# Kernel optimization log

Measured on AMD Instinct MI355X. Metric: run time of the kernel, lower is better.

## Reference

```python
import jax, jax.numpy as jnp
import numpy as np

B, C, H, W = 8, 256, 48, 48
CK = 64  # C // k
WSCALE = 0.3 / np.sqrt(C)  # keep exp(QK^T) finite (original has no 1/sqrt(d) scaling)


def conv1x1(x, w, b):
    # x: (B,C,H,W), w: (O,C,1,1), b: (O,) -> (B,O,H,W)
    return jnp.einsum('bchw,oc->bohw', x, w[:, :, 0, 0]) + b[None, :, None, None]


def setup_inputs() -> dict:
    key = jax.random.key(0)
    ks = jax.random.split(key, 6)
    x = jax.random.normal(ks[0], (B, C, H, W), dtype=jnp.float32)
    qw = jax.random.normal(ks[1], (CK, C, 1, 1), dtype=jnp.float32) * WSCALE
    kw = jax.random.normal(ks[2], (CK, C, 1, 1), dtype=jnp.float32) * WSCALE
    vw = jax.random.normal(ks[3], (C, C, 1, 1), dtype=jnp.float32) * (1.0 / np.sqrt(C))
    gw = jax.random.normal(ks[4], (C, C, 1, 1), dtype=jnp.float32) * (1.0 / np.sqrt(C))
    zk = jnp.zeros((CK,), dtype=jnp.float32)
    zc = jnp.zeros((C,), dtype=jnp.float32)
    return {
        'x': x,
        'query_weight': qw, 'query_bias': zk,
        'key_weight': kw, 'key_bias': zk,
        'value_weight': vw, 'value_bias': zc,
        'gamma_weight': gw, 'gamma_bias': zc,
        'k': 4,
    }


def reference(x, query_weight, query_bias, key_weight, key_bias,
              value_weight, value_bias, gamma_weight, gamma_bias, k):
    b, c, h, w = x.shape
    n = h * w
    q = conv1x1(x, query_weight, query_bias).reshape(b, -1, n)   # (B,Ck,N)
    kk = conv1x1(x, key_weight, key_bias).reshape(b, -1, n)      # (B,Ck,N)
    # energy[b,i,j] = q_i . k_j  (queries on rows, no sqrt(d) scaling)
    energy = jnp.einsum('bci,bcj->bij', q, kk)                   # (B,N,N)
    energy = jnp.exp(energy)
    energy = energy / jnp.sum(energy, axis=2, keepdims=True)     # unnormalized-softmax over keys
    v = conv1x1(x, value_weight, value_bias).reshape(b, c, n)    # (B,C,N)
    # out[b,c,j] = sum_i v[b,c,i] * energy[b,i,j]  (faithful to torch.bmm(V, energy))
    out = jnp.einsum('bci,bij->bcj', v, energy).reshape(b, c, h, w)
    out = conv1x1(out, gamma_weight, gamma_bias)
    return out
```

## Files before the change

kernel.cpp:

```cpp
#include <hip/hip_runtime.h>

#define BATCH 8
#define CIN   256
#define NPIX  2304
#define CKD   64
#define QKLD  128
#define NJT   (NPIX / 16)
#define NIC   (NPIX / 32)
#define KSPL  4
#define ICPS  (NIC / KSPL)
#define NJB   (NPIX / 64)

typedef _Float16 f16;
typedef __attribute__((ext_vector_type(4))) _Float16 f16x4;
typedef __attribute__((ext_vector_type(8))) _Float16 f16x8;
typedef __attribute__((ext_vector_type(4))) float    f32x4;

__global__ __launch_bounds__(256) void cast_w(
    const float* __restrict__ qw, const float* __restrict__ kw,
    const float* __restrict__ vw, const float* __restrict__ gw,
    f16* __restrict__ Wqk, f16* __restrict__ Wv, f16* __restrict__ Wg)
{
    int idx = (blockIdx.x * 256 + threadIdx.x) * 4;
    const float* src;
    f16* dst;
    if (idx < 16384)      { src = qw + idx;           dst = Wqk + idx; }
    else if (idx < 32768) { src = kw + (idx - 16384); dst = Wqk + idx; }
    else if (idx < 98304) { src = vw + (idx - 32768); dst = Wv + (idx - 32768); }
    else                  { src = gw + (idx - 98304); dst = Wg + (idx - 98304); }
    float4 v = *(const float4*)src;
    f16x4 h = { (f16)v.x, (f16)v.y, (f16)v.z, (f16)v.w };
    *(f16x4*)dst = h;
}

__global__ __launch_bounds__(256) void cast_xT(
    const float* __restrict__ x, f16* __restrict__ xT)
{
    __shared__ float s[64][65];
    const int t = threadIdx.x;
    const int n0 = blockIdx.x * 64, c0 = blockIdx.y * 64, b = blockIdx.z;
    const float* xb = x + ((size_t)b * CIN + c0) * NPIX + n0;

    const int cl = t >> 4, ng = (t & 15) * 4;
    #pragma unroll
    for (int p = 0; p < 4; ++p) {
        float4 v = *(const float4*)(xb + (size_t)(cl + 16 * p) * NPIX + ng);
        s[cl + 16 * p][ng + 0] = v.x;
        s[cl + 16 * p][ng + 1] = v.y;
        s[cl + 16 * p][ng + 2] = v.z;
        s[cl + 16 * p][ng + 3] = v.w;
    }
    __syncthreads();
    const int nl = t >> 2, cs = (t & 3) * 16;
    f16 h[16];
    #pragma unroll
    for (int j = 0; j < 16; ++j) h[j] = (f16)s[cs + j][nl];
    f16* gp = &xT[((size_t)b * NPIX + n0 + nl) * CIN + c0 + cs];
    *(f16x8*)gp       = *(f16x8*)&h[0];
    *(f16x8*)(gp + 8) = *(f16x8*)&h[8];
}

__global__ __launch_bounds__(256) void qk_conv_mfma(
    const f16* __restrict__ xT, const f16* __restrict__ Wqk,
    const float* __restrict__ qbias, const float* __restrict__ kbias,
    f16* __restrict__ qkT)
{
    const int t = threadIdx.x, w = t >> 6, lane = t & 63;
    const int quad = lane >> 4, l16 = lane & 15;
    const int wm = w & 1, wn = w >> 1;
    const int n0 = blockIdx.x * 32, b = blockIdx.y;

    const f16* bp = xT + ((size_t)b * NPIX + n0 + 16 * wn + l16) * CIN;
    const f16* ap = Wqk + (size_t)(64 * wm + l16) * CIN;

    f32x4 acc[4];
    #pragma unroll
    for (int mt = 0; mt < 4; ++mt) acc[mt] = (f32x4){0.f, 0.f, 0.f, 0.f};

    #pragma unroll
    for (int kk = 0; kk < CIN; kk += 32) {
        f16x8 bf = *(const f16x8*)(bp + kk + quad * 8);
        #pragma unroll
        for (int mt = 0; mt < 4; ++mt) {
            f16x8 af = *(const f16x8*)(ap + (size_t)mt * 16 * CIN + kk + quad * 8);
            acc[mt] = __builtin_amdgcn_mfma_f32_16x16x32_f16(af, bf, acc[mt], 0, 0, 0);
        }
    }
    const int n = n0 + 16 * wn + l16;
    const float* bias = wm ? kbias - 64 : qbias;
    #pragma unroll
    for (int mt = 0; mt < 4; ++mt) {
        int ob = 64 * wm + 16 * mt + quad * 4;
        f16x4 h;
        #pragma unroll
        for (int r = 0; r < 4; ++r)
            h[r] = (f16)(acc[mt][r] + bias[ob + r]);
        *(f16x4*)&qkT[((size_t)b * NPIX + n) * QKLD + ob] = h;
    }
}

#define ESL 136
__global__ __launch_bounds__(256) void energy_mfma(
    const f16* __restrict__ qkT, float* __restrict__ Pred,
    f16* __restrict__ Et_blk)
{
    __shared__ __align__(16) f16 es[64 * ESL];
    __shared__ float red2[2][128];
    const int t    = threadIdx.x;
    const int w    = t >> 6, lane = t & 63;
    const int quad = lane >> 4, l16 = lane & 15;
    const int j0 = blockIdx.x * 64, i0 = blockIdx.y * 128, b = blockIdx.z;
    const f16* base = qkT + (size_t)b * NPIX * QKLD;

    f32x4 acc[8];
    #pragma unroll
    for (int mt = 0; mt < 8; ++mt) acc[mt] = (f32x4){0.f, 0.f, 0.f, 0.f};

    #pragma unroll
    for (int ks = 0; ks < 2; ++ks) {
        f16x8 bf = *(const f16x8*)&base[(size_t)(j0 + 16 * w + l16) * QKLD + 64 + ks * 32 + quad * 8];
        #pragma unroll
        for (int mt = 0; mt < 8; ++mt) {
            f16x8 af = *(const f16x8*)&base[(size_t)(i0 + 16 * mt + l16) * QKLD + ks * 32 + quad * 8];
            acc[mt] = __builtin_amdgcn_mfma_f32_16x16x32_f16(af, bf, acc[mt], 0, 0, 0);
        }
    }

    #pragma unroll
    for (int mt = 0; mt < 8; ++mt) {
        f16x4 h = { (f16)__expf(acc[mt][0]), (f16)__expf(acc[mt][1]),
                    (f16)__expf(acc[mt][2]), (f16)__expf(acc[mt][3]) };
        *(f16x4*)&es[(16 * w + l16) * ESL + 16 * mt + quad * 4] = h;
    }
    __syncthreads();

    #pragma unroll
    for (int p = 0; p < 4; ++p) {
        int g  = t + 256 * p;
        int jt = g >> 8, ic = (g >> 6) & 3, ln = g & 63;
        f16x8 v = *(const f16x8*)&es[(jt * 16 + (ln & 15)) * ESL + ic * 32 + (ln >> 4) * 8];
        *(f16x8*)&Et_blk[(((size_t)b * NJT + (j0 >> 4) + jt) * NIC + (i0 >> 5) + ic) * 512 + ln * 8] = v;
    }

    {
        int i = t & 127, jq = t >> 7;
        float s = 0.f;
        #pragma unroll
        for (int jj = 0; jj < 32; ++jj)
            s += (float)es[(jq * 32 + jj) * ESL + i];
        red2[jq][i] = s;
    }
    __syncthreads();
    if (t < 128) {
        Pred[((size_t)b * NPIX + i0 + t) * NJB + blockIdx.x] =
            red2[0][t] + red2[1][t];
    }
}

__global__ __launch_bounds__(256) void reduce_S(
    const float* __restrict__ Pred, float* __restrict__ S)
{
    int idx = blockIdx.x * 256 + threadIdx.x;
    const float* p = Pred + (size_t)idx * NJB;
    float s = 0.f;
    #pragma unroll
    for (int x = 0; x < NJB; x += 4) {
        float4 v = *(const float4*)(p + x);
        s += v.x + v.y + v.z + v.w;
    }
    S[idx] = s;
}

__global__ __launch_bounds__(256) void v_conv_mfma(
    const f16* __restrict__ xT, const f16* __restrict__ Wv,
    const float* __restrict__ vbias, const float* __restrict__ S,
    f16* __restrict__ u_blk)
{
    __shared__ __align__(16) f16 smem[9216];
    f16* As = smem;
    f16* Bs = smem + 128 * 40;
    f16* us = smem;
    const int t = threadIdx.x, w = t >> 6, lane = t & 63;
    const int quad = lane >> 4, l16 = lane & 15;
    const int wm = w & 1, wn = w >> 1;
    const int i0 = blockIdx.x * 64, c0 = blockIdx.y * 128, b = blockIdx.z;
    const int sub = t >> 2, le = t & 3;
    const f16* srcA = Wv + (size_t)(c0 + sub) * CIN + le * 8;
    const f16* srcB = xT + ((size_t)b * NPIX + i0 + sub) * CIN + le * 8;
    const int ldsw = sub * 40 + le * 8;

    f32x4 acc[4][2];
    #pragma unroll
    for (int mt = 0; mt < 4; ++mt)
        #pragma unroll
        for (int nt = 0; nt < 2; ++nt)
            acc[mt][nt] = (f32x4){0.f, 0.f, 0.f, 0.f};

    for (int kk = 0; kk < CIN; kk += 32) {
        f16x8 ta0 = *(const f16x8*)(srcA + kk);
        f16x8 ta1 = *(const f16x8*)(srcA + (size_t)64 * CIN + kk);
        f16x8 tb0 = *(const f16x8*)(srcB + kk);
        __syncthreads();
        *(f16x8*)&As[ldsw]           = ta0;
        *(f16x8*)&As[64 * 40 + ldsw] = ta1;
        *(f16x8*)&Bs[ldsw]           = tb0;
        __syncthreads();
        f16x8 af[4], bf[2];
        #pragma unroll
        for (int mt = 0; mt < 4; ++mt)
            af[mt] = *(const f16x8*)&As[(64 * wm + 16 * mt + l16) * 40 + quad * 8];
        #pragma unroll
        for (int nt = 0; nt < 2; ++nt)
            bf[nt] = *(const f16x8*)&Bs[(32 * wn + 16 * nt + l16) * 40 + quad * 8];
        #pragma unroll
        for (int mt = 0; mt < 4; ++mt)
            #pragma unroll
            for (int nt = 0; nt < 2; ++nt)
                acc[mt][nt] = __builtin_amdgcn_mfma_f32_16x16x32_f16(
                    af[mt], bf[nt], acc[mt][nt], 0, 0, 0);
    }

    __syncthreads();
    #pragma unroll
    for (int nt = 0; nt < 2; ++nt) {
        int i = 32 * wn + 16 * nt + l16;
        float is = 1.0f / S[(size_t)b * NPIX + i0 + i];
        #pragma unroll
        for (int mt = 0; mt < 4; ++mt)
            #pragma unroll
            for (int r = 0; r < 4; ++r) {
                int c = 64 * wm + 16 * mt + quad * 4 + r;
                us[c * 72 + i] = (f16)((acc[mt][nt][r] + vbias[c0 + c]) * is);
            }
    }
    __syncthreads();
    #pragma unroll
    for (int p = 0; p < 4; ++p) {
        int g  = t + 256 * p;
        int ct = g >> 7, ic = (g >> 6) & 1, ln = g & 63;
        f16x8 v = *(const f16x8*)&us[(ct * 16 + (ln & 15)) * 72 + ic * 32 + (ln >> 4) * 8];
        *(f16x8*)&u_blk[(((size_t)b * 16 + (c0 >> 4) + ct) * NIC + (i0 >> 5) + ic) * 512 + ln * 8] = v;
    }
}

__global__ __launch_bounds__(512) void bmm_mfma(
    const f16* __restrict__ u_blk, const f16* __restrict__ Et_blk,
    f16* __restrict__ p0, f16* __restrict__ p1,
    f16* __restrict__ p2, f16* __restrict__ p3)
{
    const int t = threadIdx.x, w = t >> 6, lane = t & 63;
    const int quad = lane >> 4, l16 = lane & 15;
    const int wc = w & 3, wj = w >> 2;
    const int j0 = blockIdx.x * 128;
    const int ks = blockIdx.y, b = blockIdx.z;
    const f16* ub  = u_blk  + (size_t)b * 16 * NIC * 512 + (size_t)lane * 8;
    const f16* ebb = Et_blk + (size_t)b * NJT * NIC * 512 + (size_t)lane * 8;
    f16* outp = (ks == 0) ? p0 : (ks == 1 ? p1 : (ks == 2 ? p2 : p3));
    const int jtb = (j0 >> 4) + wj * 4;

    f32x4 acc[4][4];
    #pragma unroll
    for (int mt = 0; mt < 4; ++mt)
        #pragma unroll
        for (int nt = 0; nt < 4; ++nt)
            acc[mt][nt] = (f32x4){0.f, 0.f, 0.f, 0.f};

    const int ic0 = ks * ICPS;
    #pragma unroll 2
    for (int ic = ic0; ic < ic0 + ICPS; ++ic) {
        f16x8 af[4], bf[4];
        #pragma unroll
        for (int mt = 0; mt < 4; ++mt)
            af[mt] = *(const f16x8*)(ub + (size_t)((wc * 4 + mt) * NIC + ic) * 512);
        #pragma unroll
        for (int nt = 0; nt < 4; ++nt)
            bf[nt] = *(const f16x8*)(ebb + (size_t)((jtb + nt) * NIC + ic) * 512);
        #pragma unroll
        for (int mt = 0; mt < 4; ++mt)
            #pragma unroll
            for (int nt = 0; nt < 4; ++nt)
                acc[mt][nt] = __builtin_amdgcn_mfma_f32_16x16x32_f16(
                    af[mt], bf[nt], acc[mt][nt], 0, 0, 0);
    }

    #pragma unroll
    for (int mt = 0; mt < 4; ++mt) {
        int cb = (wc * 4 + mt) * 16 + quad * 4;
        #pragma unroll
        for (int nt = 0; nt < 4; ++nt) {
            int j = j0 + (wj * 4 + nt) * 16 + l16;
            f16x4 h = { (f16)acc[mt][nt][0], (f16)acc[mt][nt][1],
                        (f16)acc[mt][nt][2], (f16)acc[mt][nt][3] };
            *(f16x4*)&outp[((size_t)b * NPIX + j) * CIN + cb] = h;
        }
    }
}

__global__ __launch_bounds__(256) void gamma_conv_mfma(
    const f16* __restrict__ p0, const f16* __restrict__ p1,
    const f16* __restrict__ p2, const f16* __restrict__ p3,
    const f16* __restrict__ Wg, const float* __restrict__ gbias,
    float* __restrict__ out)
{
    __shared__ __align__(16) f16 As[128 * 40];
    __shared__ __align__(16) f16 Bs[64 * 40];
    const int t = threadIdx.x, w = t >> 6, lane = t & 63;
    const int quad = lane >> 4, l16 = lane & 15;
    const int wm = w & 1, wn = w >> 1;
    const int j0 = blockIdx.x * 64, o0 = blockIdx.y * 128, b = blockIdx.z;
    const int sub = t >> 2, le = t & 3;
    const f16* srcA  = Wg + (size_t)(o0 + sub) * CIN + le * 8;
    const size_t boff = ((size_t)b * NPIX + j0 + sub) * CIN + le * 8;
    const int ldsw = sub * 40 + le * 8;

    f32x4 acc[4][2];
    #pragma unroll
    for (int mt = 0; mt < 4; ++mt)
        #pragma unroll
        for (int nt = 0; nt < 2; ++nt)
            acc[mt][nt] = (f32x4){0.f, 0.f, 0.f, 0.f};

    for (int kk = 0; kk < CIN; kk += 32) {
        f16x8 ta0 = *(const f16x8*)(srcA + kk);
        f16x8 ta1 = *(const f16x8*)(srcA + (size_t)64 * CIN + kk);
        f16x8 tb0 = *(const f16x8*)(p0 + boff + kk);
        f16x8 tb1 = *(const f16x8*)(p1 + boff + kk);
        f16x8 tb2 = *(const f16x8*)(p2 + boff + kk);
        f16x8 tb3 = *(const f16x8*)(p3 + boff + kk);
        f16x8 tbs = (tb0 + tb1) + (tb2 + tb3);
        __syncthreads();
        *(f16x8*)&As[ldsw]           = ta0;
        *(f16x8*)&As[64 * 40 + ldsw] = ta1;
        *(f16x8*)&Bs[ldsw]           = tbs;
        __syncthreads();
        f16x8 af[4], bf[2];
        #pragma unroll
        for (int mt = 0; mt < 4; ++mt)
            af[mt] = *(const f16x8*)&As[(64 * wm + 16 * mt + l16) * 40 + quad * 8];
        #pragma unroll
        for (int nt = 0; nt < 2; ++nt)
            bf[nt] = *(const f16x8*)&Bs[(32 * wn + 16 * nt + l16) * 40 + quad * 8];
        #pragma unroll
        for (int mt = 0; mt < 4; ++mt)
            #pragma unroll
            for (int nt = 0; nt < 2; ++nt)
                acc[mt][nt] = __builtin_amdgcn_mfma_f32_16x16x32_f16(
                    af[mt], bf[nt], acc[mt][nt], 0, 0, 0);
    }

    #pragma unroll
    for (int mt = 0; mt < 4; ++mt)
        #pragma unroll
        for (int r = 0; r < 4; ++r) {
            int o = o0 + 64 * wm + 16 * mt + quad * 4 + r;
            float bv = gbias[o];
            #pragma unroll
            for (int nt = 0; nt < 2; ++nt) {
                int j = j0 + 32 * wn + 16 * nt + l16;
                out[((size_t)b * CIN + o) * NPIX + j] = acc[mt][nt][r] + bv;
            }
        }
}

extern "C" void kernel_launch(void* const* d_in, const int* in_sizes, int n_in,
                              void* d_out, int out_size, void* d_ws, size_t ws_size,
                              hipStream_t stream) {
    const float* x   = (const float*)d_in[0];
    const float* qw  = (const float*)d_in[1];
    const float* qbv = (const float*)d_in[2];
    const float* kw  = (const float*)d_in[3];
    const float* kbv = (const float*)d_in[4];
    const float* vw  = (const float*)d_in[5];
    const float* vbv = (const float*)d_in[6];
    const float* gw  = (const float*)d_in[7];
    const float* gbv = (const float*)d_in[8];
    float* out = (float*)d_out;

    const size_t BCN  = (size_t)BATCH * CIN * NPIX;
    const size_t BN   = (size_t)BATCH * NPIX;
    const size_t BNN  = (size_t)BATCH * NPIX * NPIX;
    const size_t BNQK = (size_t)BATCH * NPIX * QKLD;

    f16* Et    = (f16*)d_ws;
    f16* u_blk = Et + BNN;
    f16* xT    = u_blk + BCN;
    f16* qkT   = xT + BCN;
    f16* p1    = qkT + BNQK;
    f16* p2    = p1 + BCN;
    f16* p3    = p2 + BCN;
    f16* Wqk   = p3 + BCN;
    f16* Wv    = Wqk + 128 * 256;
    f16* Wg    = Wv + 256 * 256;
    float* S   = (float*)(Wg + 256 * 256);
    float* Pred= S + BN;
    f16* p0    = xT;

    cast_w<<<160, 256, 0, stream>>>(qw, kw, vw, gw, Wqk, Wv, Wg);
    cast_xT<<<dim3(NPIX / 64, CIN / 64, BATCH), 256, 0, stream>>>(x, xT);
    qk_conv_mfma<<<dim3(NPIX / 32, BATCH), 256, 0, stream>>>(xT, Wqk, qbv, kbv, qkT);
    energy_mfma<<<dim3(NPIX / 64, NPIX / 128, BATCH), 256, 0, stream>>>(qkT, Pred, Et);
    reduce_S<<<(int)(BN / 256), 256, 0, stream>>>(Pred, S);
    v_conv_mfma<<<dim3(NPIX / 64, CIN / 128, BATCH), 256, 0, stream>>>(xT, Wv, vbv, S, u_blk);
    bmm_mfma<<<dim3(NPIX / 128, KSPL, BATCH), 512, 0, stream>>>(u_blk, Et, p0, p1, p2, p3);
    gamma_conv_mfma<<<dim3(NPIX / 64, CIN / 128, BATCH), 256, 0, stream>>>(p0, p1, p2, p3, Wg, gbv, out);
}
```

Baseline: 228.9 us.

## Fuse energy recompute into attention bmm, drop materialized energy matrix

Instead of writing the full exp(QK^T) matrix to global memory and reading it back in a split-K bmm, the bmm kernel now recomputes energy tiles from q/k blocks on the fly, exponentiates into LDS, and multiplies by the pre-scaled V. The energy kernel only produces row sums. The K-split partial outputs and their summation in the gamma conv are removed, and Q/K are stored in MFMA-fragment blocked layout. This trades roughly 85MB of energy traffic for a second QK^T matmul and exp per tile, with a smaller grid (576 blocks) and per-iteration syncs.

After: 207.9 us. -9.2%, faster.

```diff
diff --git a/kernel.cpp b/kernel.cpp
--- a/kernel.cpp
+++ b/kernel.cpp
@@ -4,17 +4,15 @@
 #define CIN   256
 #define NPIX  2304
 #define CKD   64
-#define QKLD  128
-#define NJT   (NPIX / 16)
+#define NIT   (NPIX / 16)
 #define NIC   (NPIX / 32)
-#define KSPL  4
-#define ICPS  (NIC / KSPL)
 #define NJB   (NPIX / 64)
 
 typedef _Float16 f16;
 typedef __attribute__((ext_vector_type(4))) _Float16 f16x4;
 typedef __attribute__((ext_vector_type(8))) _Float16 f16x8;
 typedef __attribute__((ext_vector_type(4))) float    f32x4;
+
 
 __global__ __launch_bounds__(256) void cast_w(
     const float* __restrict__ qw, const float* __restrict__ kw,
@@ -63,8 +61,9 @@
 __global__ __launch_bounds__(256) void qk_conv_mfma(
     const f16* __restrict__ xT, const f16* __restrict__ Wqk,
     const float* __restrict__ qbias, const float* __restrict__ kbias,
-    f16* __restrict__ qkT)
-{
+    f16* __restrict__ q_blk, f16* __restrict__ k_blk)
+{
+    __shared__ __align__(16) f16 us[32 * 136];
     const int t = threadIdx.x, w = t >> 6, lane = t & 63;
     const int quad = lane >> 4, l16 = lane & 15;
     const int wm = w & 1, wn = w >> 1;
@@ -86,23 +85,28 @@
             acc[mt] = __builtin_amdgcn_mfma_f32_16x16x32_f16(af, bf, acc[mt], 0, 0, 0);
         }
     }
-    const int n = n0 + 16 * wn + l16;
     const float* bias = wm ? kbias - 64 : qbias;
     #pragma unroll
     for (int mt = 0; mt < 4; ++mt) {
         int ob = 64 * wm + 16 * mt + quad * 4;
-        f16x4 h;
         #pragma unroll
         for (int r = 0; r < 4; ++r)
-            h[r] = (f16)(acc[mt][r] + bias[ob + r]);
-        *(f16x4*)&qkT[((size_t)b * NPIX + n) * QKLD + ob] = h;
+            us[(16 * wn + l16) * 136 + ob + r] = (f16)(acc[mt][r] + bias[ob + r]);
+    }
+    __syncthreads();
+    {
+        int ks2 = t >> 7, nt = (t >> 6) & 1, ln = t & 63;
+        const f16* usr = &us[(nt * 16 + (ln & 15)) * 136 + ks2 * 32 + (ln >> 4) * 8];
+        size_t base = (((size_t)b * NIT + (n0 >> 4) + nt) * 2 + ks2) * 512 + ln * 8;
+        *(f16x8*)&q_blk[base] = *(const f16x8*)(usr);
+        *(f16x8*)&k_blk[base] = *(const f16x8*)(usr + 64);
     }
 }
 
 #define ESL 136
-__global__ __launch_bounds__(256) void energy_mfma(
-    const f16* __restrict__ qkT, float* __restrict__ Pred,
-    f16* __restrict__ Et_blk)
+__global__ __launch_bounds__(256) void energy_S(
+    const f16* __restrict__ q_blk, const f16* __restrict__ k_blk,
+    float* __restrict__ Pred)
 {
     __shared__ __align__(16) f16 es[64 * ESL];
     __shared__ float red2[2][128];
@@ -110,7 +114,8 @@
     const int w    = t >> 6, lane = t & 63;
     const int quad = lane >> 4, l16 = lane & 15;
     const int j0 = blockIdx.x * 64, i0 = blockIdx.y * 128, b = blockIdx.z;
-    const f16* base = qkT + (size_t)b * NPIX * QKLD;
+    const size_t ln8 = (size_t)lane * 8;
+    const f16* qb = q_blk + (size_t)b * NIT * 2 * 512 + ln8;
 
     f32x4 acc[8];
     #pragma unroll
@@ -118,10 +123,11 @@
 
     #pragma unroll
     for (int ks = 0; ks < 2; ++ks) {
-        f16x8 bf = *(const f16x8*)&base[(size_t)(j0 + 16 * w + l16) * QKLD + 64 + ks * 32 + quad * 8];
+        f16x8 bf = *(const f16x8*)(k_blk +
+            (((size_t)b * NIT + (j0 >> 4) + w) * 2 + ks) * 512 + ln8);
         #pragma unroll
         for (int mt = 0; mt < 8; ++mt) {
-            f16x8 af = *(const f16x8*)&base[(size_t)(i0 + 16 * mt + l16) * QKLD + ks * 32 + quad * 8];
+            f16x8 af = *(const f16x8*)(qb + ((size_t)((i0 >> 4) + mt) * 2 + ks) * 512);
             acc[mt] = __builtin_amdgcn_mfma_f32_16x16x32_f16(af, bf, acc[mt], 0, 0, 0);
         }
     }
@@ -133,15 +139,6 @@
         *(f16x4*)&es[(16 * w + l16) * ESL + 16 * mt + quad * 4] = h;
     }
     __syncthreads();
-
-    #pragma unroll
-    for (int p = 0; p < 4; ++p) {
-        int g  = t + 256 * p;
-        int jt = g >> 8, ic = (g >> 6) & 3, ln = g & 63;
-        f16x8 v = *(const f16x8*)&es[(jt * 16 + (ln & 15)) * ESL + ic * 32 + (ln >> 4) * 8];
-        *(f16x8*)&Et_blk[(((size_t)b * NJT + (j0 >> 4) + jt) * NIC + (i0 >> 5) + ic) * 512 + ln * 8] = v;
-    }
-
     {
         int i = t & 127, jq = t >> 7;
         float s = 0.f;
@@ -151,23 +148,20 @@
         red2[jq][i] = s;
     }
     __syncthreads();
-    if (t < 128) {
-        Pred[((size_t)b * NPIX + i0 + t) * NJB + blockIdx.x] =
+    if (t < 128)
+        Pred[((size_t)blockIdx.x * BATCH + b) * NPIX + i0 + t] =
             red2[0][t] + red2[1][t];
-    }
 }
 
 __global__ __launch_bounds__(256) void reduce_S(
     const float* __restrict__ Pred, float* __restrict__ S)
 {
-    int idx = blockIdx.x * 256 + threadIdx.x;
-    const float* p = Pred + (size_t)idx * NJB;
+    const size_t BN = (size_t)BATCH * NPIX;
+    size_t idx = (size_t)blockIdx.x * 256 + threadIdx.x;
     float s = 0.f;
     #pragma unroll
-    for (int x = 0; x < NJB; x += 4) {
-        float4 v = *(const float4*)(p + x);
-        s += v.x + v.y + v.z + v.w;
-    }
+    for (int jb = 0; jb < NJB; ++jb)
+        s += Pred[(size_t)jb * BN + idx];
     S[idx] = s;
 }
 
@@ -243,64 +237,83 @@
     }
 }
 
-__global__ __launch_bounds__(512) void bmm_mfma(
-    const f16* __restrict__ u_blk, const f16* __restrict__ Et_blk,
-    f16* __restrict__ p0, f16* __restrict__ p1,
-    f16* __restrict__ p2, f16* __restrict__ p3)
-{
+__global__ __launch_bounds__(256) void fused_bmm(
+    const f16* __restrict__ q_blk, const f16* __restrict__ k_blk,
+    const f16* __restrict__ u_blk, f16* __restrict__ o1T)
+{
+    __shared__ __align__(16) f16 es[64 * 72];
     const int t = threadIdx.x, w = t >> 6, lane = t & 63;
     const int quad = lane >> 4, l16 = lane & 15;
-    const int wc = w & 3, wj = w >> 2;
-    const int j0 = blockIdx.x * 128;
-    const int ks = blockIdx.y, b = blockIdx.z;
-    const f16* ub  = u_blk  + (size_t)b * 16 * NIC * 512 + (size_t)lane * 8;
-    const f16* ebb = Et_blk + (size_t)b * NJT * NIC * 512 + (size_t)lane * 8;
-    f16* outp = (ks == 0) ? p0 : (ks == 1 ? p1 : (ks == 2 ? p2 : p3));
-    const int jtb = (j0 >> 4) + wj * 4;
-
-    f32x4 acc[4][4];
-    #pragma unroll
-    for (int mt = 0; mt < 4; ++mt)
-        #pragma unroll
-        for (int nt = 0; nt < 4; ++nt)
-            acc[mt][nt] = (f32x4){0.f, 0.f, 0.f, 0.f};
-
-    const int ic0 = ks * ICPS;
-    #pragma unroll 2
-    for (int ic = ic0; ic < ic0 + ICPS; ++ic) {
-        f16x8 af[4], bf[4];
-        #pragma unroll
-        for (int mt = 0; mt < 4; ++mt)
-            af[mt] = *(const f16x8*)(ub + (size_t)((wc * 4 + mt) * NIC + ic) * 512);
-        #pragma unroll
-        for (int nt = 0; nt < 4; ++nt)
-            bf[nt] = *(const f16x8*)(ebb + (size_t)((jtb + nt) * NIC + ic) * 512);
-        #pragma unroll
-        for (int mt = 0; mt < 4; ++mt)
-            #pragma unroll
-            for (int nt = 0; nt < 4; ++nt)
-                acc[mt][nt] = __builtin_amdgcn_mfma_f32_16x16x32_f16(
-                    af[mt], bf[nt], acc[mt][nt], 0, 0, 0);
-    }
-
-    #pragma unroll
-    for (int mt = 0; mt < 4; ++mt) {
-        int cb = (wc * 4 + mt) * 16 + quad * 4;
-        #pragma unroll
-        for (int nt = 0; nt < 4; ++nt) {
-            int j = j0 + (wj * 4 + nt) * 16 + l16;
-            f16x4 h = { (f16)acc[mt][nt][0], (f16)acc[mt][nt][1],
-                        (f16)acc[mt][nt][2], (f16)acc[mt][nt][3] };
-            *(f16x4*)&outp[((size_t)b * NPIX + j) * CIN + cb] = h;
+    const int j0 = blockIdx.x * 64;
+    const int ch = blockIdx.y, b = blockIdx.z;
+    const size_t ln8 = (size_t)lane * 8;
+
+    const f16* qb = q_blk + (size_t)b * NIT * 2 * 512 + ln8;
+    const f16* ub = u_blk + (size_t)b * 16 * NIC * 512 + ln8;
+
+    f16x8 kf[2];
+    #pragma unroll
+    for (int ks = 0; ks < 2; ++ks)
+        kf[ks] = *(const f16x8*)(k_blk +
+            (((size_t)b * NIT + (j0 >> 4) + w) * 2 + ks) * 512 + ln8);
+
+    const int CT0 = ch * 8 + 2 * w;
+
+    f32x4 acc[2][4];
+    #pragma unroll
+    for (int mt = 0; mt < 2; ++mt)
+        #pragma unroll
+        for (int jt = 0; jt < 4; ++jt)
+            acc[mt][jt] = (f32x4){0.f, 0.f, 0.f, 0.f};
+
+    for (int ic = 0; ic < NPIX / 64; ++ic) {
+        f32x4 e[4];
+        #pragma unroll
+        for (int it = 0; it < 4; ++it) e[it] = (f32x4){0.f, 0.f, 0.f, 0.f};
+        #pragma unroll
+        for (int ks = 0; ks < 2; ++ks)
+            #pragma unroll
+            for (int it = 0; it < 4; ++it) {
+                f16x8 af = *(const f16x8*)(qb + ((size_t)(ic * 4 + it) * 2 + ks) * 512);
+                e[it] = __builtin_amdgcn_mfma_f32_16x16x32_f16(af, kf[ks], e[it], 0, 0, 0);
+            }
+        __syncthreads();
+        #pragma unroll
+        for (int it = 0; it < 4; ++it) {
+            f16x4 h = { (f16)__expf(e[it][0]), (f16)__expf(e[it][1]),
+                        (f16)__expf(e[it][2]), (f16)__expf(e[it][3]) };
+            *(f16x4*)&es[(16 * w + l16) * 72 + it * 16 + quad * 4] = h;
+        }
+        __syncthreads();
+        #pragma unroll
+        for (int isub = 0; isub < 2; ++isub) {
+            f16x8 af0 = *(const f16x8*)(ub + ((size_t)(CT0 + 0) * NIC + ic * 2 + isub) * 512);
+            f16x8 af1 = *(const f16x8*)(ub + ((size_t)(CT0 + 1) * NIC + ic * 2 + isub) * 512);
+            #pragma unroll
+            for (int jt = 0; jt < 4; ++jt) {
+                f16x8 bf = *(const f16x8*)&es[(16 * jt + l16) * 72 + isub * 32 + quad * 8];
+                acc[0][jt] = __builtin_amdgcn_mfma_f32_16x16x32_f16(af0, bf, acc[0][jt], 0, 0, 0);
+                acc[1][jt] = __builtin_amdgcn_mfma_f32_16x16x32_f16(af1, bf, acc[1][jt], 0, 0, 0);
+            }
+        }
+    }
+
+    #pragma unroll
+    for (int mt = 0; mt < 2; ++mt) {
+        int cb = ch * 128 + 32 * w + 16 * mt + quad * 4;
+        #pragma unroll
+        for (int jt = 0; jt < 4; ++jt) {
+            int j = j0 + 16 * jt + l16;
+            f16x4 h = { (f16)acc[mt][jt][0], (f16)acc[mt][jt][1],
+                        (f16)acc[mt][jt][2], (f16)acc[mt][jt][3] };
+            *(f16x4*)&o1T[((size_t)b * NPIX + j) * CIN + cb] = h;
         }
     }
 }
 
 __global__ __launch_bounds__(256) void gamma_conv_mfma(
-    const f16* __restrict__ p0, const f16* __restrict__ p1,
-    const f16* __restrict__ p2, const f16* __restrict__ p3,
-    const f16* __restrict__ Wg, const float* __restrict__ gbias,
-    float* __restrict__ out)
+    const f16* __restrict__ o1T, const f16* __restrict__ Wg,
+    const float* __restrict__ gbias, float* __restrict__ out)
 {
     __shared__ __align__(16) f16 As[128 * 40];
     __shared__ __align__(16) f16 Bs[64 * 40];
@@ -309,8 +322,8 @@
     const int wm = w & 1, wn = w >> 1;
     const int j0 = blockIdx.x * 64, o0 = blockIdx.y * 128, b = blockIdx.z;
     const int sub = t >> 2, le = t & 3;
-    const f16* srcA  = Wg + (size_t)(o0 + sub) * CIN + le * 8;
-    const size_t boff = ((size_t)b * NPIX + j0 + sub) * CIN + le * 8;
+    const f16* srcA = Wg + (size_t)(o0 + sub) * CIN + le * 8;
+    const f16* srcB = o1T + ((size_t)b * NPIX + j0 + sub) * CIN + le * 8;
     const int ldsw = sub * 40 + le * 8;
 
     f32x4 acc[4][2];
@@ -323,15 +336,11 @@
     for (int kk = 0; kk < CIN; kk += 32) {
         f16x8 ta0 = *(const f16x8*)(srcA + kk);
         f16x8 ta1 = *(const f16x8*)(srcA + (size_t)64 * CIN + kk);
-        f16x8 tb0 = *(const f16x8*)(p0 + boff + kk);
-        f16x8 tb1 = *(const f16x8*)(p1 + boff + kk);
-        f16x8 tb2 = *(const f16x8*)(p2 + boff + kk);
-        f16x8 tb3 = *(const f16x8*)(p3 + boff + kk);
-        f16x8 tbs = (tb0 + tb1) + (tb2 + tb3);
+        f16x8 tb0 = *(const f16x8*)(srcB + kk);
         __syncthreads();
         *(f16x8*)&As[ldsw]           = ta0;
         *(f16x8*)&As[64 * 40 + ldsw] = ta1;
-        *(f16x8*)&Bs[ldsw]           = tbs;
+        *(f16x8*)&Bs[ldsw]           = tb0;
         __syncthreads();
         f16x8 af[4], bf[2];
         #pragma unroll
@@ -378,29 +387,25 @@
 
     const size_t BCN  = (size_t)BATCH * CIN * NPIX;
     const size_t BN   = (size_t)BATCH * NPIX;
-    const size_t BNN  = (size_t)BATCH * NPIX * NPIX;
-    const size_t BNQK = (size_t)BATCH * NPIX * QKLD;
-
-    f16* Et    = (f16*)d_ws;
-    f16* u_blk = Et + BNN;
+    const size_t BNCK = (size_t)BATCH * NPIX * CKD;
+
+    f16* q_blk = (f16*)d_ws;
+    f16* k_blk = q_blk + BNCK;
+    f16* u_blk = k_blk + BNCK;
     f16* xT    = u_blk + BCN;
-    f16* qkT   = xT + BCN;
-    f16* p1    = qkT + BNQK;
-    f16* p2    = p1 + BCN;
-    f16* p3    = p2 + BCN;
-    f16* Wqk   = p3 + BCN;
+    f16* o1T   = xT + BCN;
+    f16* Wqk   = o1T + BCN;
     f16* Wv    = Wqk + 128 * 256;
     f16* Wg    = Wv + 256 * 256;
     float* S   = (float*)(Wg + 256 * 256);
     float* Pred= S + BN;
-    f16* p0    = xT;
 
     cast_w<<<160, 256, 0, stream>>>(qw, kw, vw, gw, Wqk, Wv, Wg);
     cast_xT<<<dim3(NPIX / 64, CIN / 64, BATCH), 256, 0, stream>>>(x, xT);
-    qk_conv_mfma<<<dim3(NPIX / 32, BATCH), 256, 0, stream>>>(xT, Wqk, qbv, kbv, qkT);
-    energy_mfma<<<dim3(NPIX / 64, NPIX / 128, BATCH), 256, 0, stream>>>(qkT, Pred, Et);
+    qk_conv_mfma<<<dim3(NPIX / 32, BATCH), 256, 0, stream>>>(xT, Wqk, qbv, kbv, q_blk, k_blk);
+    energy_S<<<dim3(NPIX / 64, NPIX / 128, BATCH), 256, 0, stream>>>(q_blk, k_blk, Pred);
     reduce_S<<<(int)(BN / 256), 256, 0, stream>>>(Pred, S);
     v_conv_mfma<<<dim3(NPIX / 64, CIN / 128, BATCH), 256, 0, stream>>>(xT, Wv, vbv, S, u_blk);
-    bmm_mfma<<<dim3(NPIX / 128, KSPL, BATCH), 512, 0, stream>>>(u_blk, Et, p0, p1, p2, p3);
-    gamma_conv_mfma<<<dim3(NPIX / 64, CIN / 128, BATCH), 256, 0, stream>>>(p0, p1, p2, p3, Wg, gbv, out);
-}
+    fused_bmm<<<dim3(NPIX / 64, 2, BATCH), 256, 0, stream>>>(q_blk, k_blk, u_blk, o1T);
+    gamma_conv_mfma<<<dim3(NPIX / 64, CIN / 128, BATCH), 256, 0, stream>>>(o1T, Wg, gbv, out);
+}
```
